# Performance work log

Hardware: AMD Instinct MI355X
Metric: run time of the kernel (lower is better)

## Reference

```python
import jax, jax.numpy as jnp
import numpy as np
import math


def setup_inputs() -> dict:
    key = jax.random.key(0)
    kq, kk, kv, km = jax.random.split(key, 4)
    B, Lq, Lk, D = 4, 4096, 4096, 64
    queries = jax.random.normal(kq, (B, Lq, D), dtype=jnp.float32)
    keys = jax.random.normal(kk, (B, Lk, D), dtype=jnp.float32)
    values = jax.random.normal(kv, (B, Lk, D), dtype=jnp.float32)
    masks = jax.random.randint(km, (B, Lk), 0, 2, dtype=jnp.int32)
    return {"queries": queries, "keys": keys, "values": values, "masks": masks}


def reference(queries, keys, values, masks):
    # scale = sqrt(d_k) (self.scale is None)
    d_k = queries.shape[-1]
    scale = math.sqrt(d_k)
    # scores: [B, Lq, Lk]
    scores = jnp.einsum('bqd,bkd->bqk', queries, keys) / jnp.asarray(scale, queries.dtype)
    # key-padding mask [B, Lk] -> broadcast over Lq; masked positions -> -inf
    neg_inf = jnp.asarray(float('-inf'), scores.dtype)
    scores = jnp.where(masks[:, None, :] == 0, neg_inf, scores)
    attn = jax.nn.softmax(scores, axis=-1)  # dropout p=0 -> identity
    return jnp.einsum('bqk,bkd->bqd', attn, values)
```

## Files before the change

### kernel.cpp

```cpp
#include <hip/hip_runtime.h>


#define B_N    4
#define L      4096
#define DH     64
#define TILE_K 64
#define KPAD   72
#define SPLIT  8
#define SLAB   (L / SPLIT)
#define TILES  (SLAB / TILE_K)
#define QSCALE 0.18033688f

typedef unsigned short ushort8_ma __attribute__((ext_vector_type(8), may_alias));
typedef unsigned short ushort4_ma __attribute__((ext_vector_type(4), may_alias));
typedef float          f32x4_ma   __attribute__((ext_vector_type(4), may_alias));
typedef short          short8     __attribute__((ext_vector_type(8)));
typedef float          f32x16     __attribute__((ext_vector_type(16)));
typedef unsigned int   uint2_ev   __attribute__((ext_vector_type(2)));

union v8cast  { ushort8_ma u; short8 s; };
union pk4cast { unsigned int u[4]; short8 s; };

static __device__ __forceinline__ short8 ld8(const unsigned short* p) {
    v8cast x; x.u = *(const ushort8_ma*)p; return x.s;
}
static __device__ __forceinline__ unsigned short bf16rne(float f) {
    union { float f; unsigned u; } x; x.f = f;
    unsigned r = x.u + 0x7fffu + ((x.u >> 16) & 1u);
    return (unsigned short)(r >> 16);
}
static __device__ __forceinline__ float bf16tof(unsigned short u) {
    union { unsigned u; float f; } x; x.u = (unsigned)u << 16; return x.f;
}
static __device__ __forceinline__ float fast_exp2(float x) {
    return __builtin_amdgcn_exp2f(x);
}
static __device__ __forceinline__ unsigned cvt_pk_bf16(float lo, float hi) {
    unsigned r;
    asm("v_cvt_pk_bf16_f32 %0, %1, %2" : "=v"(r) : "v"(lo), "v"(hi));
    return r;
}

__global__ __launch_bounds__(256)
void prepass3(const float* __restrict__ Q, const float* __restrict__ K,
              const float* __restrict__ V, const int* __restrict__ M,
              unsigned short* __restrict__ Qb, unsigned short* __restrict__ Kb,
              unsigned short* __restrict__ Vt)
{
    __shared__ unsigned short t[64][20];
    const int b  = blockIdx.y;
    const int r0 = blockIdx.x * 16;
    const size_t base = ((size_t)b * L + r0) * DH;

    {
        int i = threadIdx.x;
        int row = i >> 4, d0 = (i & 15) * 4;
        size_t off = base + (size_t)row * DH + d0;
        f32x4_ma q = *(const f32x4_ma*)(Q + off);
        f32x4_ma k = *(const f32x4_ma*)(K + off);
        f32x4_ma v = *(const f32x4_ma*)(V + off);
        const float zf = (M[(size_t)b * L + r0 + row] == 0) ? 0.f : 1.f;
        ushort4_ma qo, ko;
        #pragma unroll
        for (int j = 0; j < 4; ++j) {
            qo[j] = bf16rne(q[j] * QSCALE);
            ko[j] = bf16rne(k[j] * zf);
            t[d0 + j][row] = bf16rne(v[j] * zf);
        }
        *(ushort4_ma*)(Qb + off) = qo;
        *(ushort4_ma*)(Kb + off) = ko;
    }
    __syncthreads();
    {
        int i = threadIdx.x;
        int d = i >> 2, k4 = (i & 3) * 4;
        ushort4_ma vo = { t[d][k4], t[d][k4 + 1], t[d][k4 + 2], t[d][k4 + 3] };
        *(ushort4_ma*)(Vt + ((size_t)b * DH + d) * L + r0 + k4) = vo;
    }
}

__global__ __launch_bounds__(256, 4)
void fa_split32(const unsigned short* __restrict__ Qb,
                const unsigned short* __restrict__ Kb,
                const unsigned short* __restrict__ Vt,
                const int*            __restrict__ Mk,
                unsigned short* __restrict__ ACCp, float* __restrict__ Lp)
{
    __shared__ unsigned short Kl[TILE_K * KPAD];
    __shared__ unsigned short Vl[DH * KPAD];
    __shared__ int            cntw[4];

    const int tid  = threadIdx.x;
    const int wave = tid >> 6;
    const int lane = tid & 63;
    const int l32  = lane & 31;
    const int hw   = lane >> 5;

    const int b      = blockIdx.y & (B_N - 1);
    const int slab   = blockIdx.y >> 2;
    const int qblock = blockIdx.x * 128;
    const int kbase  = slab * SLAB;

    short8 bQ[4];
    {
        const unsigned short* qp = Qb + ((size_t)b * L + qblock + wave * 32 + l32) * DH;
        #pragma unroll
        for (int kk = 0; kk < 4; ++kk)
            bQ[kk] = ld8(qp + kk * 16 + hw * 8);
    }

    const unsigned short* Kbb = Kb + (size_t)b * L * DH;
    const unsigned short* Vtb = Vt + (size_t)b * DH * L;
    const int*            Mb  = Mk + (size_t)b * L;

    const int c1 = tid + 256;
    const int r0 = tid >> 3, d0 = (tid & 7) * 8;
    const int r1 = c1 >> 3,  d1 = (c1 & 7) * 8;

    ushort8_ma kr0, kr1, vr0, vr1;

    kr0 = *(const ushort8_ma*)(Kbb + (size_t)(kbase + r0) * DH + d0);
    kr1 = *(const ushort8_ma*)(Kbb + (size_t)(kbase + r1) * DH + d1);
    vr0 = *(const ushort8_ma*)(Vtb + (size_t)r0 * L + kbase + d0);
    vr1 = *(const ushort8_ma*)(Vtb + (size_t)r1 * L + kbase + d1);
    const int m0 = Mb[kbase + 2 * tid];
    const int m1 = Mb[kbase + 2 * tid + 1];
    *(ushort8_ma*)(&Kl[r0 * KPAD + d0]) = kr0;
    *(ushort8_ma*)(&Kl[r1 * KPAD + d1]) = kr1;
    *(ushort8_ma*)(&Vl[r0 * KPAD + d0]) = vr0;
    *(ushort8_ma*)(&Vl[r1 * KPAD + d1]) = vr1;
    {
        unsigned long long bm0 = __ballot(m0 == 0);
        unsigned long long bm1 = __ballot(m1 == 0);
        if (lane == 0) cntw[wave] = __popcll(bm0) + __popcll(bm1);
    }
    __syncthreads();

    f32x16 acc0 = {0}, acc1 = {0};
    float rs0 = 0.f, rs1 = 0.f, rs2 = 0.f, rs3 = 0.f;

    for (int t = 0; t < TILES; ++t) {
        if (t < TILES - 1) {
            const int k0n = kbase + (t + 1) * TILE_K;
            kr0 = *(const ushort8_ma*)(Kbb + (size_t)(k0n + r0) * DH + d0);
            kr1 = *(const ushort8_ma*)(Kbb + (size_t)(k0n + r1) * DH + d1);
            vr0 = *(const ushort8_ma*)(Vtb + (size_t)r0 * L + k0n + d0);
            vr1 = *(const ushort8_ma*)(Vtb + (size_t)r1 * L + k0n + d1);
        }

        #pragma unroll
        for (int g = 0; g < 2; ++g) {
            f32x16 s = {0};
            #pragma unroll
            for (int kk = 0; kk < 4; ++kk) {
                short8 aK = ld8(&Kl[(g * 32 + l32) * KPAD + kk * 16 + hw * 8]);
                s = __builtin_amdgcn_mfma_f32_32x32x16_bf16(aK, bQ[kk], s, 0, 0, 0);
            }
            f32x16 p;
            #pragma unroll
            for (int r = 0; r < 16; r += 4) {
                p[r + 0] = fast_exp2(s[r + 0]); rs0 += p[r + 0];
                p[r + 1] = fast_exp2(s[r + 1]); rs1 += p[r + 1];
                p[r + 2] = fast_exp2(s[r + 2]); rs2 += p[r + 2];
                p[r + 3] = fast_exp2(s[r + 3]); rs3 += p[r + 3];
            }
            #pragma unroll
            for (int h = 0; h < 2; ++h) {
                const int kk = 2 * g + h;
                const int b0 = 8 * h;
                unsigned A0 = cvt_pk_bf16(p[b0 + 0], p[b0 + 1]);
                unsigned A1 = cvt_pk_bf16(p[b0 + 2], p[b0 + 3]);
                unsigned B0 = cvt_pk_bf16(p[b0 + 4], p[b0 + 5]);
                unsigned B1 = cvt_pk_bf16(p[b0 + 6], p[b0 + 7]);
                uint2_ev r02 = __builtin_amdgcn_permlane32_swap(A0, B0, false, false);
                uint2_ev r13 = __builtin_amdgcn_permlane32_swap(A1, B1, false, false);
                pk4cast P;
                P.u[0] = r02[0]; P.u[1] = r13[0];
                P.u[2] = r02[1]; P.u[3] = r13[1];
                short8 bV0 = ld8(&Vl[l32 * KPAD + kk * 16 + hw * 8]);
                acc0 = __builtin_amdgcn_mfma_f32_32x32x16_bf16(P.s, bV0, acc0, 0, 0, 0);
                short8 bV1 = ld8(&Vl[(32 + l32) * KPAD + kk * 16 + hw * 8]);
                acc1 = __builtin_amdgcn_mfma_f32_32x32x16_bf16(P.s, bV1, acc1, 0, 0, 0);
            }
        }

        __syncthreads();
        if (t < TILES - 1) {
            *(ushort8_ma*)(&Kl[r0 * KPAD + d0]) = kr0;
            *(ushort8_ma*)(&Kl[r1 * KPAD + d1]) = kr1;
            *(ushort8_ma*)(&Vl[r0 * KPAD + d0]) = vr0;
            *(ushort8_ma*)(&Vl[r1 * KPAD + d1]) = vr1;
            __syncthreads();
        }
    }

    float rs = (rs0 + rs1) + (rs2 + rs3);
    rs += __shfl_xor(rs, 32);
    const float scnt = (float)(cntw[0] + cntw[1] + cntw[2] + cntw[3]);
    const size_t pbase = ((size_t)(slab * B_N + b)) * L;
    #pragma unroll
    for (int reg = 0; reg < 16; ++reg) {
        int row  = (reg & 3) + 8 * (reg >> 2) + 4 * hw;
        int qrow = qblock + wave * 32 + row;
        unsigned short* ap = ACCp + (pbase + qrow) * DH;
        ap[l32]      = bf16rne(acc0[reg]);
        ap[32 + l32] = bf16rne(acc1[reg]);
    }
    if (hw == 0)
        Lp[pbase + qblock + wave * 32 + l32] = rs - scnt;
}

__global__ __launch_bounds__(256)
void fa_combine(const unsigned short* __restrict__ ACCp,
                const float* __restrict__ Lp, float* __restrict__ O)
{
    const int b    = blockIdx.y;
    const int qrow = blockIdx.x * 4 + (threadIdx.x >> 6);
    const int d    = threadIdx.x & 63;

    float lsum = 0.f, o = 0.f;
    #pragma unroll
    for (int s = 0; s < SPLIT; ++s) {
        lsum += Lp[((size_t)(s * B_N + b)) * L + qrow];
        o    += bf16tof(ACCp[(((size_t)(s * B_N + b)) * L + qrow) * DH + d]);
    }
    O[((size_t)b * L + qrow) * DH + d] = o / fmaxf(lsum, 1e-20f);
}

#define TK  64
#define RW  4
#define RB  16
#define KST 67

__global__ __launch_bounds__(256)
void fa_scalar(const float* __restrict__ Q, const float* __restrict__ K,
               const float* __restrict__ V, const int* __restrict__ Mk,
               float* __restrict__ O)
{
    __shared__ float Kt[TK][KST];
    __shared__ float Vts[DH][KST];
    __shared__ float Qs[RB][DH];
    __shared__ float Ps[4][RW][TK];
    __shared__ float Bs[TK];

    const int tid = threadIdx.x, w = tid >> 6, lane = tid & 63;
    const int b = blockIdx.y, row0 = blockIdx.x * RB;

    for (int i = tid; i < RB * DH; i += 256) {
        int r = i >> 6, d = i & 63;
        Qs[r][d] = Q[((size_t)b * L + row0 + r) * DH + d];
    }
    float m[RW], l[RW], acc[RW];
    #pragma unroll
    for (int rr = 0; rr < RW; ++rr) { m[rr] = -1e30f; l[rr] = 0.f; acc[rr] = 0.f; }

    for (int k0 = 0; k0 < L; k0 += TK) {
        __syncthreads();
        for (int i = tid; i < TK * DH; i += 256) {
            int key = i >> 6, d = i & 63;
            Kt[key][d]  = K[((size_t)b * L + k0 + key) * DH + d];
            Vts[d][key] = V[((size_t)b * L + k0 + key) * DH + d];
        }
        if (tid < TK) Bs[tid] = (Mk[(size_t)b * L + k0 + tid] == 0) ? -1e30f : 0.f;
        __syncthreads();
        float s[RW];
        #pragma unroll
        for (int rr = 0; rr < RW; ++rr) s[rr] = 0.f;
        for (int d4 = 0; d4 < DH; d4 += 4) {
            float kv[4];
            #pragma unroll
            for (int j = 0; j < 4; ++j) kv[j] = Kt[lane][d4 + j];
            #pragma unroll
            for (int rr = 0; rr < RW; ++rr)
                #pragma unroll
                for (int j = 0; j < 4; ++j)
                    s[rr] += Qs[w * RW + rr][d4 + j] * kv[j];
        }
        float alpha[RW];
        #pragma unroll
        for (int rr = 0; rr < RW; ++rr) {
            float sv = s[rr] * 0.125f + Bs[lane];
            float t = sv;
            #pragma unroll
            for (int off = 1; off < 64; off <<= 1) t = fmaxf(t, __shfl_xor(t, off));
            float mnew = fmaxf(m[rr], t);
            alpha[rr] = __expf(fminf(m[rr] - mnew, 0.f));
            float p = __expf(fminf(sv - mnew, 0.f));
            Ps[w][rr][lane] = p;
            float su = p;
            #pragma unroll
            for (int off = 1; off < 64; off <<= 1) su += __shfl_xor(su, off);
            l[rr] = l[rr] * alpha[rr] + su;
            m[rr] = mnew;
        }
        __syncthreads();
        #pragma unroll
        for (int rr = 0; rr < RW; ++rr) acc[rr] *= alpha[rr];
        for (int k4 = 0; k4 < TK; k4 += 4) {
            float vv[4];
            #pragma unroll
            for (int j = 0; j < 4; ++j) vv[j] = Vts[lane][k4 + j];
            #pragma unroll
            for (int rr = 0; rr < RW; ++rr)
                #pragma unroll
                for (int j = 0; j < 4; ++j)
                    acc[rr] += Ps[w][rr][k4 + j] * vv[j];
        }
    }
    #pragma unroll
    for (int rr = 0; rr < RW; ++rr) {
        int row = row0 + w * RW + rr;
        O[((size_t)b * L + row) * DH + lane] = acc[rr] / fmaxf(l[rr], 1e-20f);
    }
}

extern "C" void kernel_launch(void* const* d_in, const int* in_sizes, int n_in,
                              void* d_out, int out_size, void* d_ws, size_t ws_size,
                              hipStream_t stream) {
    const float* Q = (const float*)d_in[0];
    const float* K = (const float*)d_in[1];
    const float* V = (const float*)d_in[2];
    const int*   M = (const int*)d_in[3];
    float*       O = (float*)d_out;

    const size_t elems     = (size_t)B_N * L * DH;
    const size_t bf16_need = elems * 2 * 3;
    const size_t acc_elems = (size_t)SPLIT * B_N * L * DH;
    const size_t ml_elems  = (size_t)SPLIT * B_N * L;
    const size_t full_need = bf16_need + acc_elems * 2 + ml_elems * 4;

    unsigned short* Qb = (unsigned short*)d_ws;
    unsigned short* Kb = Qb + elems;
    unsigned short* Vt = Kb + elems;

    if (ws_size >= full_need) {
        unsigned short* ACCp = Vt + elems;
        float*          Lp   = (float*)(ACCp + acc_elems);

        prepass3<<<dim3(L / 16, B_N), dim3(256), 0, stream>>>(Q, K, V, M, Qb, Kb, Vt);
        fa_split32<<<dim3(L / 128, B_N * SPLIT), dim3(256), 0, stream>>>(
            Qb, Kb, Vt, M, ACCp, Lp);
        fa_combine<<<dim3(L / 4, B_N), dim3(256), 0, stream>>>(ACCp, Lp, O);
    } else {
        fa_scalar<<<dim3(L / RB, B_N), dim3(256), 0, stream>>>(Q, K, V, M, O);
    }
}
```

Measured before the change: 94.90 us.

## Process 64 query rows per wave to reuse K/V LDS fragments

Each wave now handles two 32-row query tiles, so every K fragment read from LDS feeds two QK MFMAs and every V fragment feeds two PV MFMAs. The block covers 256 query rows and the grid halves, cutting LDS traffic and global K/V tile loads per query. The cost is doubled accumulator and Q register use (launch bounds lowered to 2 blocks per CU) and only 512 blocks, which lowers occupancy and may leave CUs underused.

```diff
diff --git a/kernel.cpp b/kernel.cpp
--- a/kernel.cpp
+++ b/kernel.cpp
@@ -39,6 +39,18 @@
     unsigned r;
     asm("v_cvt_pk_bf16_f32 %0, %1, %2" : "=v"(r) : "v"(lo), "v"(hi));
     return r;
+}
+static __device__ __forceinline__ short8 build_P(const f32x16& p, int b0) {
+    unsigned A0 = cvt_pk_bf16(p[b0 + 0], p[b0 + 1]);
+    unsigned A1 = cvt_pk_bf16(p[b0 + 2], p[b0 + 3]);
+    unsigned B0 = cvt_pk_bf16(p[b0 + 4], p[b0 + 5]);
+    unsigned B1 = cvt_pk_bf16(p[b0 + 6], p[b0 + 7]);
+    uint2_ev r02 = __builtin_amdgcn_permlane32_swap(A0, B0, false, false);
+    uint2_ev r13 = __builtin_amdgcn_permlane32_swap(A1, B1, false, false);
+    pk4cast P;
+    P.u[0] = r02[0]; P.u[1] = r13[0];
+    P.u[2] = r02[1]; P.u[3] = r13[1];
+    return P.s;
 }
 
 __global__ __launch_bounds__(256)
@@ -79,8 +91,8 @@
     }
 }
 
-__global__ __launch_bounds__(256, 4)
-void fa_split32(const unsigned short* __restrict__ Qb,
+__global__ __launch_bounds__(256, 2)
+void fa_split64(const unsigned short* __restrict__ Qb,
                 const unsigned short* __restrict__ Kb,
                 const unsigned short* __restrict__ Vt,
                 const int*            __restrict__ Mk,
@@ -98,15 +110,18 @@
 
     const int b      = blockIdx.y & (B_N - 1);
     const int slab   = blockIdx.y >> 2;
-    const int qblock = blockIdx.x * 128;
+    const int qblock = blockIdx.x * 256;
     const int kbase  = slab * SLAB;
-
-    short8 bQ[4];
+    const int qbase  = qblock + wave * 64;
+
+    short8 q00, q01, q02, q03, q10, q11, q12, q13;
     {
-        const unsigned short* qp = Qb + ((size_t)b * L + qblock + wave * 32 + l32) * DH;
-        #pragma unroll
-        for (int kk = 0; kk < 4; ++kk)
-            bQ[kk] = ld8(qp + kk * 16 + hw * 8);
+        const unsigned short* qp0 = Qb + ((size_t)b * L + qbase + l32) * DH + hw * 8;
+        const unsigned short* qp1 = qp0 + 32 * DH;
+        q00 = ld8(qp0);      q01 = ld8(qp0 + 16);
+        q02 = ld8(qp0 + 32); q03 = ld8(qp0 + 48);
+        q10 = ld8(qp1);      q11 = ld8(qp1 + 16);
+        q12 = ld8(qp1 + 32); q13 = ld8(qp1 + 48);
     }
 
     const unsigned short* Kbb = Kb + (size_t)b * L * DH;
@@ -118,6 +133,7 @@
     const int r1 = c1 >> 3,  d1 = (c1 & 7) * 8;
 
     ushort8_ma kr0, kr1, vr0, vr1;
+    int mr_unused = 0; (void)mr_unused;
 
     kr0 = *(const ushort8_ma*)(Kbb + (size_t)(kbase + r0) * DH + d0);
     kr1 = *(const ushort8_ma*)(Kbb + (size_t)(kbase + r1) * DH + d1);
@@ -136,8 +152,9 @@
     }
     __syncthreads();
 
-    f32x16 acc0 = {0}, acc1 = {0};
-    float rs0 = 0.f, rs1 = 0.f, rs2 = 0.f, rs3 = 0.f;
+    f32x16 a00 = {0}, a01 = {0}, a10 = {0}, a11 = {0};
+    float rA0 = 0.f, rA1 = 0.f, rA2 = 0.f, rA3 = 0.f;
+    float rB0 = 0.f, rB1 = 0.f, rB2 = 0.f, rB3 = 0.f;
 
     for (int t = 0; t < TILES; ++t) {
         if (t < TILES - 1) {
@@ -150,37 +167,49 @@
 
         #pragma unroll
         for (int g = 0; g < 2; ++g) {
-            f32x16 s = {0};
-            #pragma unroll
-            for (int kk = 0; kk < 4; ++kk) {
-                short8 aK = ld8(&Kl[(g * 32 + l32) * KPAD + kk * 16 + hw * 8]);
-                s = __builtin_amdgcn_mfma_f32_32x32x16_bf16(aK, bQ[kk], s, 0, 0, 0);
+            const unsigned short* kp = &Kl[(g * 32 + l32) * KPAD + hw * 8];
+            short8 aK0 = ld8(kp);
+            short8 aK1 = ld8(kp + 16);
+            short8 aK2 = ld8(kp + 32);
+            short8 aK3 = ld8(kp + 48);
+
+            f32x16 s0 = {0}, s1 = {0};
+            s0 = __builtin_amdgcn_mfma_f32_32x32x16_bf16(aK0, q00, s0, 0, 0, 0);
+            s1 = __builtin_amdgcn_mfma_f32_32x32x16_bf16(aK0, q10, s1, 0, 0, 0);
+            s0 = __builtin_amdgcn_mfma_f32_32x32x16_bf16(aK1, q01, s0, 0, 0, 0);
+            s1 = __builtin_amdgcn_mfma_f32_32x32x16_bf16(aK1, q11, s1, 0, 0, 0);
+            s0 = __builtin_amdgcn_mfma_f32_32x32x16_bf16(aK2, q02, s0, 0, 0, 0);
+            s1 = __builtin_amdgcn_mfma_f32_32x32x16_bf16(aK2, q12, s1, 0, 0, 0);
+            s0 = __builtin_amdgcn_mfma_f32_32x32x16_bf16(aK3, q03, s0, 0, 0, 0);
+            s1 = __builtin_amdgcn_mfma_f32_32x32x16_bf16(aK3, q13, s1, 0, 0, 0);
+
+            f32x16 p0, p1;
+            #pragma unroll
+            for (int r = 0; r < 16; r += 4) {
+                p0[r + 0] = fast_exp2(s0[r + 0]); rA0 += p0[r + 0];
+                p0[r + 1] = fast_exp2(s0[r + 1]); rA1 += p0[r + 1];
+                p0[r + 2] = fast_exp2(s0[r + 2]); rA2 += p0[r + 2];
+                p0[r + 3] = fast_exp2(s0[r + 3]); rA3 += p0[r + 3];
             }
-            f32x16 p;
             #pragma unroll
             for (int r = 0; r < 16; r += 4) {
-                p[r + 0] = fast_exp2(s[r + 0]); rs0 += p[r + 0];
-                p[r + 1] = fast_exp2(s[r + 1]); rs1 += p[r + 1];
-                p[r + 2] = fast_exp2(s[r + 2]); rs2 += p[r + 2];
-                p[r + 3] = fast_exp2(s[r + 3]); rs3 += p[r + 3];
+                p1[r + 0] = fast_exp2(s1[r + 0]); rB0 += p1[r + 0];
+                p1[r + 1] = fast_exp2(s1[r + 1]); rB1 += p1[r + 1];
+                p1[r + 2] = fast_exp2(s1[r + 2]); rB2 += p1[r + 2];
+                p1[r + 3] = fast_exp2(s1[r + 3]); rB3 += p1[r + 3];
             }
             #pragma unroll
             for (int h = 0; h < 2; ++h) {
                 const int kk = 2 * g + h;
-                const int b0 = 8 * h;
-                unsigned A0 = cvt_pk_bf16(p[b0 + 0], p[b0 + 1]);
-                unsigned A1 = cvt_pk_bf16(p[b0 + 2], p[b0 + 3]);
-                unsigned B0 = cvt_pk_bf16(p[b0 + 4], p[b0 + 5]);
-                unsigned B1 = cvt_pk_bf16(p[b0 + 6], p[b0 + 7]);
-                uint2_ev r02 = __builtin_amdgcn_permlane32_swap(A0, B0, false, false);
-                uint2_ev r13 = __builtin_amdgcn_permlane32_swap(A1, B1, false, false);
-                pk4cast P;
-                P.u[0] = r02[0]; P.u[1] = r13[0];
-                P.u[2] = r02[1]; P.u[3] = r13[1];
-                short8 bV0 = ld8(&Vl[l32 * KPAD + kk * 16 + hw * 8]);
-                acc0 = __builtin_amdgcn_mfma_f32_32x32x16_bf16(P.s, bV0, acc0, 0, 0, 0);
-                short8 bV1 = ld8(&Vl[(32 + l32) * KPAD + kk * 16 + hw * 8]);
-                acc1 = __builtin_amdgcn_mfma_f32_32x32x16_bf16(P.s, bV1, acc1, 0, 0, 0);
+                const unsigned short* vp = &Vl[l32 * KPAD + kk * 16 + hw * 8];
+                short8 bV0 = ld8(vp);
+                short8 bV1 = ld8(vp + 32 * KPAD);
+                short8 P0 = build_P(p0, 8 * h);
+                a00 = __builtin_amdgcn_mfma_f32_32x32x16_bf16(P0, bV0, a00, 0, 0, 0);
+                a01 = __builtin_amdgcn_mfma_f32_32x32x16_bf16(P0, bV1, a01, 0, 0, 0);
+                short8 P1 = build_P(p1, 8 * h);
+                a10 = __builtin_amdgcn_mfma_f32_32x32x16_bf16(P1, bV0, a10, 0, 0, 0);
+                a11 = __builtin_amdgcn_mfma_f32_32x32x16_bf16(P1, bV1, a11, 0, 0, 0);
             }
         }
 
@@ -194,20 +223,26 @@
         }
     }
 
-    float rs = (rs0 + rs1) + (rs2 + rs3);
-    rs += __shfl_xor(rs, 32);
+    float rsA = (rA0 + rA1) + (rA2 + rA3);
+    float rsB = (rB0 + rB1) + (rB2 + rB3);
+    rsA += __shfl_xor(rsA, 32);
+    rsB += __shfl_xor(rsB, 32);
     const float scnt = (float)(cntw[0] + cntw[1] + cntw[2] + cntw[3]);
     const size_t pbase = ((size_t)(slab * B_N + b)) * L;
     #pragma unroll
     for (int reg = 0; reg < 16; ++reg) {
-        int row  = (reg & 3) + 8 * (reg >> 2) + 4 * hw;
-        int qrow = qblock + wave * 32 + row;
-        unsigned short* ap = ACCp + (pbase + qrow) * DH;
-        ap[l32]      = bf16rne(acc0[reg]);
-        ap[32 + l32] = bf16rne(acc1[reg]);
-    }
-    if (hw == 0)
-        Lp[pbase + qblock + wave * 32 + l32] = rs - scnt;
+        int row = (reg & 3) + 8 * (reg >> 2) + 4 * hw;
+        unsigned short* ap0 = ACCp + (pbase + qbase + row) * DH;
+        unsigned short* ap1 = ACCp + (pbase + qbase + 32 + row) * DH;
+        ap0[l32]      = bf16rne(a00[reg]);
+        ap0[32 + l32] = bf16rne(a01[reg]);
+        ap1[l32]      = bf16rne(a10[reg]);
+        ap1[32 + l32] = bf16rne(a11[reg]);
+    }
+    if (hw == 0) {
+        Lp[pbase + qbase + l32]      = rsA - scnt;
+        Lp[pbase + qbase + 32 + l32] = rsB - scnt;
+    }
 }
 
 __global__ __launch_bounds__(256)
@@ -338,7 +373,7 @@
         float*          Lp   = (float*)(ACCp + acc_elems);
 
         prepass3<<<dim3(L / 16, B_N), dim3(256), 0, stream>>>(Q, K, V, M, Qb, Kb, Vt);
-        fa_split32<<<dim3(L / 128, B_N * SPLIT), dim3(256), 0, stream>>>(
+        fa_split64<<<dim3(L / 256, B_N * SPLIT), dim3(256), 0, stream>>>(
             Qb, Kb, Vt, M, ACCp, Lp);
         fa_combine<<<dim3(L / 4, B_N), dim3(256), 0, stream>>>(ACCp, Lp, O);
     } else {
```

New measurement: 93.29 us. About the same (-1.7%).
